# Kernel tuning notes

Measured on AMD Instinct MI355X. Metric: run time of the kernel, lower is better.

The kernel has to match this reference:

```python
import jax, jax.numpy as jnp
import numpy as np

LN_EPS = 1e-5  # torch nn.LayerNorm default
L2_EPS = 1e-12  # F.normalize default


def layer_norm(x, gamma, beta):
    mu = jnp.mean(x, axis=-1, keepdims=True)
    var = jnp.mean(jnp.square(x - mu), axis=-1, keepdims=True)
    return (x - mu) * jax.lax.rsqrt(var + LN_EPS) * gamma + beta


def l2_normalize(x):
    n = jnp.linalg.norm(x, axis=-1, keepdims=True)
    return x / jnp.maximum(n, L2_EPS)


def setup_inputs() -> dict:
    key = jax.random.key(0)
    k_x, k_mu = jax.random.split(key, 2)
    B, C, H, W = 4, 512, 128, 128
    K, M = 19, 5  # num_classes, num_components_per_class
    x = jax.random.normal(k_x, (B, C, H, W), dtype=jnp.float32)
    means = 0.02 * jax.random.normal(k_mu, (K, M, C), dtype=jnp.float32)  # trunc_normal_(std=0.02)
    diagonal = jnp.ones((K, M, C), dtype=jnp.float32)
    feat_gamma = jnp.ones((C,), dtype=jnp.float32)
    feat_beta = jnp.zeros((C,), dtype=jnp.float32)
    mask_gamma = jnp.ones((K,), dtype=jnp.float32)
    mask_beta = jnp.zeros((K,), dtype=jnp.float32)
    return dict(x=x, means=means, diagonal=diagonal,
                feat_gamma=feat_gamma, feat_beta=feat_beta,
                mask_gamma=mask_gamma, mask_beta=mask_beta)


def reference(x, means, diagonal, feat_gamma, feat_beta, mask_gamma, mask_beta):
    B, C, H, W = x.shape
    K, M, D = means.shape
    # rearrange 'b c h w -> (b h w) c'
    f = jnp.transpose(x, (0, 2, 3, 1)).reshape(-1, C)  # (N, D)
    f = layer_norm(f, feat_gamma, feat_beta)
    f = l2_normalize(f)
    # means are re-normalized in-place each forward
    mu = l2_normalize(means).reshape(K * M, D)          # (P, D), P = K*M
    sigma = diagonal.reshape(K * M, D)                  # diagonal scale (std)
    inv_var = 1.0 / jnp.square(sigma)
    # Mahalanobis distance via quadratic expansion (avoids (N,P,D) intermediate):
    # sum_d ((f - mu)/sigma)^2 = f^2 . iv - 2 f . (mu*iv) + sum(mu^2 * iv)
    q1 = jnp.square(f) @ inv_var.T                      # (N, P)
    q2 = f @ (mu * inv_var).T                           # (N, P)
    q3 = jnp.sum(jnp.square(mu) * inv_var, axis=-1)     # (P,)
    maha = q1 - 2.0 * q2 + q3[None, :]
    log_det = jnp.sum(jnp.log(sigma), axis=-1)          # sum log sigma, (P,)
    half_log2pi = 0.5 * D * jnp.log(2.0 * jnp.pi)
    log_prob = -0.5 * maha - log_det[None, :] - half_log2pi  # (N, P)
    log_prob = log_prob.reshape(-1, K, M)
    m_prob = jnp.max(log_prob, axis=-1)                 # amax over components, (N, K)
    out = layer_norm(m_prob, mask_gamma, mask_beta)
    # rearrange '(b h w) k -> b k h w'
    out_seg = jnp.transpose(out.reshape(B, H, W, K), (0, 3, 1, 2))
    return out_seg
```

## Files before the change

kernel.cpp:

```cpp
#include <hip/hip_runtime.h>
#include <math.h>

#define C_ 512
#define HW_ 16384
#define K_ 19
#define M_ 5
#define P_ 95
#define P2 96
#define TPX 64
#define NBLK 1024
#define HL2PI 470.49652900081467f

typedef __attribute__((ext_vector_type(8))) short short8;
typedef __attribute__((ext_vector_type(4))) int int4v;
typedef __attribute__((ext_vector_type(4))) float float4v;

static __device__ __forceinline__ short f2bf(float f) {
  unsigned u = __builtin_bit_cast(unsigned, f);
  unsigned r = (u + 0x7fffu + ((u >> 16) & 1u)) >> 16;
  return (short)r;
}

static __device__ __forceinline__ int pk2(float a, float b) {
  int r;
  asm("v_cvt_pk_bf16_f32 %0, %1, %2" : "=v"(r) : "v"(a), "v"(b));
  return r;
}

static __device__ __forceinline__ short8 sq8(short8 a) {
  int4v ai = __builtin_bit_cast(int4v, a);
  int4v ri;
#pragma unroll
  for (int j = 0; j < 4; j++) {
    unsigned u = (unsigned)ai[j];
    float lo = __builtin_bit_cast(float, u << 16);
    float hi = __builtin_bit_cast(float, u & 0xffff0000u);
    ri[j] = pk2(lo * lo, hi * hi);
  }
  return __builtin_bit_cast(short8, ri);
}

__device__ __forceinline__ float block_reduce_sum(float v, volatile float* red) {
#pragma unroll
  for (int o = 32; o; o >>= 1) v += __shfl_down(v, o);
  const int lane = threadIdx.x & 63, wv = threadIdx.x >> 6;
  if (lane == 0) red[wv] = v;
  __syncthreads();
  float r = red[0] + red[1] + red[2] + red[3];
  __syncthreads();
  return r;
}

__global__ __launch_bounds__(256) void prep_kernel(
    const float* __restrict__ means, const float* __restrict__ diag,
    short* __restrict__ wbf, float* __restrict__ cterm) {
  const int p = blockIdx.x;
  const int tid = threadIdx.x;
  __shared__ float red[4];
  if (p >= P_) {
    for (int c = tid; c < C_; c += 256) {
      wbf[p * 1024 + c] = 0;
      wbf[p * 1024 + 512 + c] = 0;
    }
    if (tid == 0) cterm[p] = 0.f;
    return;
  }
  const float* mrow = means + (size_t)p * C_;
  const float* srow = diag + (size_t)p * C_;
  float m0 = mrow[tid], m1 = mrow[tid + 256];
  float ss = block_reduce_sum(m0 * m0 + m1 * m1, red);
  float rden = 1.f / fmaxf(sqrtf(ss), 1e-12f);
  float q3 = 0.f, ld = 0.f;
#pragma unroll
  for (int t = 0; t < 2; t++) {
    int c = tid + t * 256;
    float m = mrow[c], s = srow[c];
    float mu = m * rden;
    float iv = 1.f / (s * s);
    wbf[p * 1024 + c] = f2bf(iv);
    wbf[p * 1024 + 512 + c] = f2bf(mu * iv);
    q3 += mu * mu * iv;
    ld += logf(s);
  }
  q3 = block_reduce_sum(q3, red);
  ld = block_reduce_sum(ld, red);
  if (tid == 0) cterm[p] = -0.5f * q3 - ld - HL2PI;
}

__global__ __launch_bounds__(512, 4) void main_kernel(
    const float* __restrict__ x,
    const float* __restrict__ fg, const float* __restrict__ fb,
    const float* __restrict__ mg, const float* __restrict__ mb,
    const short* __restrict__ wbf, const float* __restrict__ cterm,
    float* __restrict__ out) {
  __shared__ __align__(16) char raw[65536];
  __shared__ float red0[8 * TPX], red1[8 * TPX];
  __shared__ float meanA[TPX], rstdA[TPX], rnA[TPX], rn2A[TPX];
  __shared__ float mean2A[TPX], rstd2A[TPX];
  __shared__ float mpr[TPX * 20];

  const int tid = threadIdx.x;
  const int px = tid & 63;
  const int part = tid >> 6;
  const int lane = tid & 63;
  const int n0 = blockIdx.x * TPX;
  const int b = n0 >> 14;
  const int rem = n0 & 16383;
  const int h = rem >> 7;
  const int w0 = rem & 127;
  const int cbase = part * 64;
  const float* xp = x + (size_t)b * C_ * HW_ + h * 128 + w0 + px;

  float xr[64];
#pragma unroll
  for (int i = 0; i < 64; i++) xr[i] = xp[(size_t)(cbase + i) * HW_];
  {
    float s = 0.f, q = 0.f;
#pragma unroll
    for (int i = 0; i < 64; i++) {
      s += xr[i];
      q += xr[i] * xr[i];
    }
    red0[part * 64 + px] = s;
    red1[part * 64 + px] = q;
  }
  __syncthreads();
  if (tid < 64) {
    float ss = 0.f, qq = 0.f;
#pragma unroll
    for (int i = 0; i < 8; i++) {
      ss += red0[i * 64 + tid];
      qq += red1[i * 64 + tid];
    }
    float mean = ss * (1.f / C_);
    float var = qq * (1.f / C_) - mean * mean;
    meanA[tid] = mean;
    rstdA[tid] = rsqrtf(var + 1e-5f);
  }
  __syncthreads();

  {
    const float mean = meanA[px], rstd = rstdA[px];
    const int t_ = px >> 4, lq = px & 15;
    float s2 = 0.f;
#pragma unroll
    for (int t8 = 0; t8 < 8; t8++) {
      const int c0 = cbase + t8 * 8;
      float vv[8];
#pragma unroll
      for (int j = 0; j < 8; j++) {
        float v = fmaf((xr[t8 * 8 + j] - mean) * rstd, fg[c0 + j], fb[c0 + j]);
        s2 += v * v;
        vv[j] = v;
      }
      int4v pk;
#pragma unroll
      for (int j2 = 0; j2 < 4; j2++) pk[j2] = pk2(vv[2 * j2], vv[2 * j2 + 1]);
      *(int4v*)(raw + (((t_ * 16 + (c0 >> 5)) << 10) | (((c0 >> 3) & 3) << 8) | (lq << 4))) = pk;
    }
    red0[part * 64 + px] = s2;
  }
  __syncthreads();
  if (tid < 64) {
    float ss = 0.f;
#pragma unroll
    for (int i = 0; i < 8; i++) ss += red0[i * 64 + tid];
    float rn = 1.f / fmaxf(sqrtf(ss), 1e-12f);
    rnA[tid] = rn;
    rn2A[tid] = rn * rn;
  }
  __syncthreads();

  const int wv = part;
  const int khalf = wv >> 2;
  const int pbase = ((wv >> 1) & 1) * 3;
  const int pxpair = wv & 1;
  const int lm = lane & 15, lk = lane >> 4;
  float4v acc[3][2] = {{}, {}, {}};
  const short* wrow = wbf + (((pbase * 16 + lm) << 10) + (khalf << 9) + (lk << 3));
  const int base0 = (pxpair * 2) * 16384;
  const int base1 = (pxpair * 2 + 1) * 16384;
#pragma unroll 4
  for (int ksl = 0; ksl < 16; ksl++) {
    short8 a0 = *(const short8*)(wrow + ksl * 32);
    short8 a1 = *(const short8*)(wrow + 16384 + ksl * 32);
    short8 a2 = *(const short8*)(wrow + 32768 + ksl * 32);
    short8 b0 = *(const short8*)(raw + base0 + (ksl << 10) + (lane << 4));
    short8 b1 = *(const short8*)(raw + base1 + (ksl << 10) + (lane << 4));
    if (khalf == 0) {
      b0 = sq8(b0);
      b1 = sq8(b1);
    }
    acc[0][0] = __builtin_amdgcn_mfma_f32_16x16x32_bf16(a0, b0, acc[0][0], 0, 0, 0);
    acc[0][1] = __builtin_amdgcn_mfma_f32_16x16x32_bf16(a0, b1, acc[0][1], 0, 0, 0);
    acc[1][0] = __builtin_amdgcn_mfma_f32_16x16x32_bf16(a1, b0, acc[1][0], 0, 0, 0);
    acc[1][1] = __builtin_amdgcn_mfma_f32_16x16x32_bf16(a1, b1, acc[1][1], 0, 0, 0);
    acc[2][0] = __builtin_amdgcn_mfma_f32_16x16x32_bf16(a2, b0, acc[2][0], 0, 0, 0);
    acc[2][1] = __builtin_amdgcn_mfma_f32_16x16x32_bf16(a2, b1, acc[2][1], 0, 0, 0);
  }
  __syncthreads();
  float* lp = (float*)raw;

  if (khalf == 0) {
#pragma unroll
    for (int i = 0; i < 3; i++) {
      const int prow = (pbase + i) * 16 + lk * 4;
#pragma unroll
      for (int r = 0; r < 4; r++) {
        const float ct = cterm[prow + r];
#pragma unroll
        for (int t2 = 0; t2 < 2; t2++) {
          const int pxx = (pxpair * 2 + t2) * 16 + lm;
          lp[pxx * 100 + prow + r] = fmaf(-0.5f * rn2A[pxx], acc[i][t2][r], ct);
        }
      }
    }
  }
  __syncthreads();
  if (khalf == 1) {
#pragma unroll
    for (int i = 0; i < 3; i++) {
      const int prow = (pbase + i) * 16 + lk * 4;
#pragma unroll
      for (int r = 0; r < 4; r++) {
#pragma unroll
        for (int t2 = 0; t2 < 2; t2++) {
          const int pxx = (pxpair * 2 + t2) * 16 + lm;
          lp[pxx * 100 + prow + r] += rnA[pxx] * acc[i][t2][r];
        }
      }
    }
  }
  __syncthreads();

  for (int idx = tid; idx < TPX * K_; idx += 512) {
    const int pxx = idx / K_;
    const int k = idx - pxx * K_;
    const float* row = lp + pxx * 100 + k * M_;
    float mv = row[0];
#pragma unroll
    for (int m = 1; m < M_; m++) mv = fmaxf(mv, row[m]);
    mpr[pxx * 20 + k] = mv;
  }
  __syncthreads();
  if (tid < 64) {
    float ss = 0.f;
    for (int k = 0; k < K_; k++) ss += mpr[tid * 20 + k];
    float m2 = ss * (1.f / K_);
    float qq = 0.f;
    for (int k = 0; k < K_; k++) {
      float d = mpr[tid * 20 + k] - m2;
      qq += d * d;
    }
    mean2A[tid] = m2;
    rstd2A[tid] = rsqrtf(qq * (1.f / K_) + 1e-5f);
  }
  __syncthreads();
  float* obase = out + ((size_t)(b * K_) * 128 + h) * 128 + w0;
  for (int idx = tid; idx < TPX * K_; idx += 512) {
    const int k = idx >> 6, pxx = idx & 63;
    float v = fmaf((mpr[pxx * 20 + k] - mean2A[pxx]) * rstd2A[pxx], mg[k], mb[k]);
    obase[(size_t)k * HW_ + pxx] = v;
  }
}

extern "C" void kernel_launch(void* const* d_in, const int* in_sizes, int n_in,
                              void* d_out, int out_size, void* d_ws, size_t ws_size,
                              hipStream_t stream) {
  const float* x = (const float*)d_in[0];
  const float* means = (const float*)d_in[1];
  const float* diag = (const float*)d_in[2];
  const float* fg = (const float*)d_in[3];
  const float* fb = (const float*)d_in[4];
  const float* mg = (const float*)d_in[5];
  const float* mb = (const float*)d_in[6];
  float* out = (float*)d_out;

  short* wbf = (short*)d_ws;
  float* cterm = (float*)((char*)d_ws + (size_t)P2 * 1024 * 2);

  prep_kernel<<<P2, 256, 0, stream>>>(means, diag, wbf, cterm);
  main_kernel<<<NBLK, 512, 0, stream>>>(x, fg, fb, mg, mb, wbf, cterm, out);
}
```

Baseline: 76.21 us.

## Restructure main kernel as single-wave blocks over 16 pixels with register-resident features

The 512-thread, 64-pixel block is replaced by a 64-thread block that handles 16 pixels. Each lane keeps its channel slice packed as bf16 in registers, and the two norm reductions become cross-lane shuffles instead of LDS round-trips and block barriers. The wave computes both the squared-feature and mean products for all 96 components itself, and a single wave does the amax and output layer norm. This removes most LDS staging and synchronisation. In exchange, each wave rereads the full weight matrix for only 16 pixels, so L2 weight traffic is four times higher, global loads cover only 64-byte contiguous runs per channel, and the grid has half as many waves in total. Raw x is also rounded to bf16 before the layer norm is applied, which slightly lowers precision.

New measurement: 154.9 us. +103.3%, slower.

```diff
diff --git a/kernel.cpp b/kernel.cpp
--- a/kernel.cpp
+++ b/kernel.cpp
@@ -7,8 +7,7 @@
 #define M_ 5
 #define P_ 95
 #define P2 96
-#define TPX 64
-#define NBLK 1024
+#define NT_ 4096
 #define HL2PI 470.49652900081467f
 
 typedef __attribute__((ext_vector_type(8))) short short8;
@@ -20,13 +19,11 @@
   unsigned r = (u + 0x7fffu + ((u >> 16) & 1u)) >> 16;
   return (short)r;
 }
-
 static __device__ __forceinline__ int pk2(float a, float b) {
   int r;
   asm("v_cvt_pk_bf16_f32 %0, %1, %2" : "=v"(r) : "v"(a), "v"(b));
   return r;
 }
-
 static __device__ __forceinline__ short8 sq8(short8 a) {
   int4v ai = __builtin_bit_cast(int4v, a);
   int4v ri;
@@ -87,180 +84,145 @@
   if (tid == 0) cterm[p] = -0.5f * q3 - ld - HL2PI;
 }
 
-__global__ __launch_bounds__(512, 4) void main_kernel(
+__global__ __launch_bounds__(64, 3) void main_kernel(
     const float* __restrict__ x,
     const float* __restrict__ fg, const float* __restrict__ fb,
     const float* __restrict__ mg, const float* __restrict__ mb,
     const short* __restrict__ wbf, const float* __restrict__ cterm,
     float* __restrict__ out) {
-  __shared__ __align__(16) char raw[65536];
-  __shared__ float red0[8 * TPX], red1[8 * TPX];
-  __shared__ float meanA[TPX], rstdA[TPX], rnA[TPX], rn2A[TPX];
-  __shared__ float mean2A[TPX], rstd2A[TPX];
-  __shared__ float mpr[TPX * 20];
-
-  const int tid = threadIdx.x;
-  const int px = tid & 63;
-  const int part = tid >> 6;
-  const int lane = tid & 63;
-  const int n0 = blockIdx.x * TPX;
+  __shared__ float fgs[C_], fbs[C_], cts[P2], mgs[20], mbs[20];
+  __shared__ float lp[16 * 100];
+
+  const int lane = threadIdx.x;
+  const int pxl = lane & 15, q_ = lane >> 4;
+
+  for (int i = lane; i < C_; i += 64) {
+    fgs[i] = fg[i];
+    fbs[i] = fb[i];
+  }
+  for (int i = lane; i < P2; i += 64) cts[i] = cterm[i];
+  if (lane < K_) {
+    mgs[lane] = mg[lane];
+    mbs[lane] = mb[lane];
+  }
+
+  const int n0 = blockIdx.x * 16;
   const int b = n0 >> 14;
   const int rem = n0 & 16383;
   const int h = rem >> 7;
   const int w0 = rem & 127;
-  const int cbase = part * 64;
-  const float* xp = x + (size_t)b * C_ * HW_ + h * 128 + w0 + px;
-
-  float xr[64];
-#pragma unroll
-  for (int i = 0; i < 64; i++) xr[i] = xp[(size_t)(cbase + i) * HW_];
-  {
-    float s = 0.f, q = 0.f;
-#pragma unroll
-    for (int i = 0; i < 64; i++) {
-      s += xr[i];
-      q += xr[i] * xr[i];
-    }
-    red0[part * 64 + px] = s;
-    red1[part * 64 + px] = q;
-  }
-  __syncthreads();
-  if (tid < 64) {
-    float ss = 0.f, qq = 0.f;
-#pragma unroll
-    for (int i = 0; i < 8; i++) {
-      ss += red0[i * 64 + tid];
-      qq += red1[i * 64 + tid];
-    }
-    float mean = ss * (1.f / C_);
-    float var = qq * (1.f / C_) - mean * mean;
-    meanA[tid] = mean;
-    rstdA[tid] = rsqrtf(var + 1e-5f);
-  }
-  __syncthreads();
-
-  {
-    const float mean = meanA[px], rstd = rstdA[px];
-    const int t_ = px >> 4, lq = px & 15;
-    float s2 = 0.f;
-#pragma unroll
-    for (int t8 = 0; t8 < 8; t8++) {
-      const int c0 = cbase + t8 * 8;
-      float vv[8];
-#pragma unroll
-      for (int j = 0; j < 8; j++) {
-        float v = fmaf((xr[t8 * 8 + j] - mean) * rstd, fg[c0 + j], fb[c0 + j]);
-        s2 += v * v;
-        vv[j] = v;
-      }
-      int4v pk;
-#pragma unroll
-      for (int j2 = 0; j2 < 4; j2++) pk[j2] = pk2(vv[2 * j2], vv[2 * j2 + 1]);
-      *(int4v*)(raw + (((t_ * 16 + (c0 >> 5)) << 10) | (((c0 >> 3) & 3) << 8) | (lq << 4))) = pk;
-    }
-    red0[part * 64 + px] = s2;
-  }
-  __syncthreads();
-  if (tid < 64) {
-    float ss = 0.f;
-#pragma unroll
-    for (int i = 0; i < 8; i++) ss += red0[i * 64 + tid];
-    float rn = 1.f / fmaxf(sqrtf(ss), 1e-12f);
-    rnA[tid] = rn;
-    rn2A[tid] = rn * rn;
-  }
-  __syncthreads();
-
-  const int wv = part;
-  const int khalf = wv >> 2;
-  const int pbase = ((wv >> 1) & 1) * 3;
-  const int pxpair = wv & 1;
-  const int lm = lane & 15, lk = lane >> 4;
-  float4v acc[3][2] = {{}, {}, {}};
-  const short* wrow = wbf + (((pbase * 16 + lm) << 10) + (khalf << 9) + (lk << 3));
-  const int base0 = (pxpair * 2) * 16384;
-  const int base1 = (pxpair * 2 + 1) * 16384;
-#pragma unroll 4
-  for (int ksl = 0; ksl < 16; ksl++) {
-    short8 a0 = *(const short8*)(wrow + ksl * 32);
-    short8 a1 = *(const short8*)(wrow + 16384 + ksl * 32);
-    short8 a2 = *(const short8*)(wrow + 32768 + ksl * 32);
-    short8 b0 = *(const short8*)(raw + base0 + (ksl << 10) + (lane << 4));
-    short8 b1 = *(const short8*)(raw + base1 + (ksl << 10) + (lane << 4));
-    if (khalf == 0) {
-      b0 = sq8(b0);
-      b1 = sq8(b1);
-    }
-    acc[0][0] = __builtin_amdgcn_mfma_f32_16x16x32_bf16(a0, b0, acc[0][0], 0, 0, 0);
-    acc[0][1] = __builtin_amdgcn_mfma_f32_16x16x32_bf16(a0, b1, acc[0][1], 0, 0, 0);
-    acc[1][0] = __builtin_amdgcn_mfma_f32_16x16x32_bf16(a1, b0, acc[1][0], 0, 0, 0);
-    acc[1][1] = __builtin_amdgcn_mfma_f32_16x16x32_bf16(a1, b1, acc[1][1], 0, 0, 0);
-    acc[2][0] = __builtin_amdgcn_mfma_f32_16x16x32_bf16(a2, b0, acc[2][0], 0, 0, 0);
-    acc[2][1] = __builtin_amdgcn_mfma_f32_16x16x32_bf16(a2, b1, acc[2][1], 0, 0, 0);
-  }
-  __syncthreads();
-  float* lp = (float*)raw;
-
-  if (khalf == 0) {
-#pragma unroll
-    for (int i = 0; i < 3; i++) {
-      const int prow = (pbase + i) * 16 + lk * 4;
-#pragma unroll
-      for (int r = 0; r < 4; r++) {
-        const float ct = cterm[prow + r];
-#pragma unroll
-        for (int t2 = 0; t2 < 2; t2++) {
-          const int pxx = (pxpair * 2 + t2) * 16 + lm;
-          lp[pxx * 100 + prow + r] = fmaf(-0.5f * rn2A[pxx], acc[i][t2][r], ct);
-        }
-      }
-    }
-  }
-  __syncthreads();
-  if (khalf == 1) {
-#pragma unroll
-    for (int i = 0; i < 3; i++) {
-      const int prow = (pbase + i) * 16 + lk * 4;
-#pragma unroll
-      for (int r = 0; r < 4; r++) {
-#pragma unroll
-        for (int t2 = 0; t2 < 2; t2++) {
-          const int pxx = (pxpair * 2 + t2) * 16 + lm;
-          lp[pxx * 100 + prow + r] += rnA[pxx] * acc[i][t2][r];
-        }
-      }
-    }
-  }
-  __syncthreads();
-
-  for (int idx = tid; idx < TPX * K_; idx += 512) {
-    const int pxx = idx / K_;
-    const int k = idx - pxx * K_;
-    const float* row = lp + pxx * 100 + k * M_;
-    float mv = row[0];
-#pragma unroll
-    for (int m = 1; m < M_; m++) mv = fmaxf(mv, row[m]);
-    mpr[pxx * 20 + k] = mv;
-  }
-  __syncthreads();
-  if (tid < 64) {
-    float ss = 0.f;
-    for (int k = 0; k < K_; k++) ss += mpr[tid * 20 + k];
-    float m2 = ss * (1.f / K_);
-    float qq = 0.f;
-    for (int k = 0; k < K_; k++) {
-      float d = mpr[tid * 20 + k] - m2;
-      qq += d * d;
-    }
-    mean2A[tid] = m2;
-    rstd2A[tid] = rsqrtf(qq * (1.f / K_) + 1e-5f);
-  }
-  __syncthreads();
-  float* obase = out + ((size_t)(b * K_) * 128 + h) * 128 + w0;
-  for (int idx = tid; idx < TPX * K_; idx += 512) {
-    const int k = idx >> 6, pxx = idx & 63;
-    float v = fmaf((mpr[pxx * 20 + k] - mean2A[pxx]) * rstd2A[pxx], mg[k], mb[k]);
-    obase[(size_t)k * HW_ + pxx] = v;
+  const float* xb = x + (size_t)b * C_ * HW_ + h * 128 + w0 + pxl;
+  const int cq = q_ * 8;
+
+  int pxv[64];
+  float s = 0.f, sq = 0.f;
+#pragma unroll
+  for (int t = 0; t < 16; t++) {
+    float xv[8];
+#pragma unroll
+    for (int j = 0; j < 8; j++) xv[j] = xb[(size_t)(t * 32 + cq + j) * HW_];
+#pragma unroll
+    for (int j = 0; j < 8; j++) {
+      s += xv[j];
+      sq = fmaf(xv[j], xv[j], sq);
+    }
+#pragma unroll
+    for (int d = 0; d < 4; d++) pxv[t * 4 + d] = pk2(xv[2 * d], xv[2 * d + 1]);
+  }
+  s += __shfl_xor(s, 16);
+  s += __shfl_xor(s, 32);
+  sq += __shfl_xor(sq, 16);
+  sq += __shfl_xor(sq, 32);
+  const float mean = s * (1.f / C_);
+  const float var = sq * (1.f / C_) - mean * mean;
+  const float rstd = rsqrtf(var + 1e-5f);
+
+  float s2 = 0.f;
+#pragma unroll
+  for (int t = 0; t < 16; t++) {
+    const int c0 = t * 32 + cq;
+    float ga[8], ba[8];
+    *(float4v*)(ga) = *(const float4v*)(fgs + c0);
+    *(float4v*)(ga + 4) = *(const float4v*)(fgs + c0 + 4);
+    *(float4v*)(ba) = *(const float4v*)(fbs + c0);
+    *(float4v*)(ba + 4) = *(const float4v*)(fbs + c0 + 4);
+#pragma unroll
+    for (int d = 0; d < 4; d++) {
+      unsigned u = (unsigned)pxv[t * 4 + d];
+      float xlo = __builtin_bit_cast(float, u << 16);
+      float xhi = __builtin_bit_cast(float, u & 0xffff0000u);
+      float vlo = fmaf((xlo - mean) * rstd, ga[2 * d], ba[2 * d]);
+      float vhi = fmaf((xhi - mean) * rstd, ga[2 * d + 1], ba[2 * d + 1]);
+      s2 = fmaf(vlo, vlo, fmaf(vhi, vhi, s2));
+      pxv[t * 4 + d] = pk2(vlo, vhi);
+    }
+  }
+  s2 += __shfl_xor(s2, 16);
+  s2 += __shfl_xor(s2, 32);
+  const float rn = 1.f / fmaxf(sqrtf(s2), 1e-12f);
+  const float rn2 = rn * rn;
+
+  float4v aq1[6] = {}, aq2[6] = {};
+  const short* wbase = wbf + ((lane & 15) << 10) + ((lane >> 4) << 3);
+#pragma unroll
+  for (int ks = 0; ks < 16; ks++) {
+    short8 bv = __builtin_bit_cast(short8, *(int4v*)(pxv + ks * 4));
+    short8 b2 = sq8(bv);
+#pragma unroll
+    for (int pt = 0; pt < 6; pt++) {
+      const short* wr = wbase + pt * 16384 + ks * 32;
+      short8 aiv = *(const short8*)wr;
+      short8 amv = *(const short8*)(wr + 512);
+      aq1[pt] = __builtin_amdgcn_mfma_f32_16x16x32_bf16(aiv, b2, aq1[pt], 0, 0, 0);
+      aq2[pt] = __builtin_amdgcn_mfma_f32_16x16x32_bf16(amv, bv, aq2[pt], 0, 0, 0);
+    }
+  }
+
+#pragma unroll
+  for (int pt = 0; pt < 6; pt++) {
+#pragma unroll
+    for (int r = 0; r < 4; r++) {
+      const int p = pt * 16 + q_ * 4 + r;
+      lp[pxl * 100 + p] = fmaf(-0.5f * rn2, aq1[pt][r], fmaf(rn, aq2[pt][r], cts[p]));
+    }
+  }
+
+  float mk[5];
+  float sum = 0.f;
+#pragma unroll
+  for (int i = 0; i < 5; i++) {
+    const int k = q_ + 4 * i;
+    if (k < K_) {
+      const float* row = lp + pxl * 100 + k * M_;
+      float mv = fmaxf(fmaxf(row[0], row[1]), fmaxf(row[2], row[3]));
+      mv = fmaxf(mv, row[4]);
+      mk[i] = mv;
+      sum += mv;
+    } else {
+      mk[i] = 0.f;
+    }
+  }
+  sum += __shfl_xor(sum, 16);
+  sum += __shfl_xor(sum, 32);
+  const float m2 = sum * (1.f / K_);
+  float qq = 0.f;
+#pragma unroll
+  for (int i = 0; i < 5; i++) {
+    const int k = q_ + 4 * i;
+    if (k < K_) {
+      float d = mk[i] - m2;
+      qq = fmaf(d, d, qq);
+    }
+  }
+  qq += __shfl_xor(qq, 16);
+  qq += __shfl_xor(qq, 32);
+  const float rstd2 = rsqrtf(qq * (1.f / K_) + 1e-5f);
+
+  float* ob = out + (size_t)(b * K_) * HW_ + h * 128 + w0 + pxl;
+#pragma unroll
+  for (int i = 0; i < 5; i++) {
+    const int k = q_ + 4 * i;
+    if (k < K_) ob[(size_t)k * HW_] = fmaf((mk[i] - m2) * rstd2, mgs[k], mbs[k]);
   }
 }
 
@@ -280,5 +242,5 @@
   float* cterm = (float*)((char*)d_ws + (size_t)P2 * 1024 * 2);
 
   prep_kernel<<<P2, 256, 0, stream>>>(means, diag, wbf, cterm);
-  main_kernel<<<NBLK, 512, 0, stream>>>(x, fg, fb, mg, mb, wbf, cterm, out);
-}
+  main_kernel<<<NT_, 64, 0, stream>>>(x, fg, fb, mg, mb, wbf, cterm, out);
+}
```
